# Kernel optimization log

Hardware: AMD Instinct MI355X
Metric: run time of the kernel (lower is better)

## Reference

```python
import jax, jax.numpy as jnp
import numpy as np

DIM = 256
NUM_HEADS = 8
HEAD_DIM = DIM // NUM_HEADS
WH, WW = 7, 7
N = WH * WW              # tokens per window = 49
NUM_WINDOWS = 64         # windows per image (56x56 map / 7x7 windows)
B_TOTAL = 2048           # num_windows * B_images
SCALE = HEAD_DIM ** -0.5


def _relative_position_index():
    # Matches the tf.meshgrid (xy indexing) construction in the source.
    coords = np.stack(np.meshgrid(np.arange(WH), np.arange(WW)), axis=0)  # [2, WW, WH]
    flat = coords.reshape(2, -1)                                          # [2, N]
    rel = flat[:, :, None] - flat[:, None, :]                             # [2, N, N]
    rel = rel.transpose(1, 2, 0).astype(np.int32)                         # [N, N, 2]
    rel[:, :, 0] += WH - 1
    rel[:, :, 1] += WW - 1
    rel[:, :, 0] *= 2 * WW - 1
    return rel.sum(-1)                                                    # [N, N]


def setup_inputs() -> dict:
    key = jax.random.key(0)
    ks = jax.random.split(key, 6)
    std = 0.02
    x = jax.random.normal(ks[0], (B_TOTAL, N, DIM), dtype=jnp.float32)
    mask = jnp.zeros((NUM_WINDOWS, N, N), dtype=jnp.float32)  # 0 / -inf additive mask
    qkv_w = jax.random.normal(ks[1], (DIM, 3 * DIM), dtype=jnp.float32) * std
    qkv_b = jnp.zeros((3 * DIM,), dtype=jnp.float32)
    proj_w = jax.random.normal(ks[2], (DIM, DIM), dtype=jnp.float32) * std
    proj_b = jnp.zeros((DIM,), dtype=jnp.float32)
    n_rel = (2 * WH - 1) * (2 * WW - 1)  # 169
    bias_table = jax.random.normal(ks[3], (n_rel, NUM_HEADS), dtype=jnp.float32) * std
    rel_index = jnp.asarray(_relative_position_index(), dtype=jnp.int32)
    return {"x": x, "mask": mask, "qkv_w": qkv_w, "qkv_b": qkv_b,
            "proj_w": proj_w, "proj_b": proj_b, "bias_table": bias_table,
            "rel_index": rel_index}


def reference(x, mask, qkv_w, qkv_b, proj_w, proj_b, bias_table, rel_index):
    B = x.shape[0]
    # qkv projection -> [3, B, H, N, hd]
    qkv = x @ qkv_w + qkv_b                                  # [B, N, 3C]
    qkv = qkv.reshape(B, N, 3, NUM_HEADS, HEAD_DIM)
    qkv = jnp.transpose(qkv, (2, 0, 3, 1, 4))
    q, k, v = qkv[0], qkv[1], qkv[2]
    # scaled attention scores [B, H, N, N]
    attn = jnp.einsum('bhnd,bhmd->bhnm', q, k) * SCALE
    # relative position bias gather: [N*N] -> [N, N, H] -> [1, H, N, N]
    bias = bias_table[rel_index.reshape(-1)].reshape(N, N, NUM_HEADS)
    attn = attn + jnp.transpose(bias, (2, 0, 1))[None]
    # additive window mask [nW, N, N]
    nW = mask.shape[0]
    attn = attn.reshape(B // nW, nW, NUM_HEADS, N, N) + mask[None, :, None]
    attn = attn.reshape(B, NUM_HEADS, N, N)
    attn = jax.nn.softmax(attn, axis=-1)
    out = jnp.einsum('bhnm,bhmd->bhnd', attn, v)             # [B, H, N, hd]
    out = jnp.transpose(out, (0, 2, 1, 3)).reshape(B, N, DIM)
    return out @ proj_w + proj_b
```

## Files before the change

kernel.cpp:

```cpp
#include <hip/hip_runtime.h>

#define NTOK 49
#define NHEAD 8
#define HDIM 32
#define DIMC 256
#define SCALE_F 0.17677669529663687f

typedef __attribute__((ext_vector_type(8))) short short8;
typedef __attribute__((ext_vector_type(4))) float f32x4;

#define AS1P(p) ((__attribute__((address_space(1))) void*)(p))
#define AS3P(p) ((__attribute__((address_space(3))) void*)(p))

__device__ inline unsigned short f2bf(float f) {
    unsigned int u = __float_as_uint(f);
    u += 0x7fffu + ((u >> 16) & 1u);
    return (unsigned short)(u >> 16);
}

__global__ __launch_bounds__(256) void conv_pack(const float* __restrict__ in,
    unsigned short* __restrict__ xp, int M)
{
    __shared__ __align__(16) unsigned short T[32 * 64 * 8];
    const int t = threadIdx.x;
    const size_t m0 = (size_t)blockIdx.x * 64;
    const float* src = in + m0 * 256;
    #pragma unroll
    for (int i = 0; i < 8; ++i) {
        const int li = i * 256 + t;
        const int r  = li >> 5;
        const int kc = li & 31;
        float4 a = ((const float4*)src)[li * 2];
        float4 b = ((const float4*)src)[li * 2 + 1];
        union { unsigned short s[8]; uint4 v; } u;
        u.s[0] = f2bf(a.x); u.s[1] = f2bf(a.y); u.s[2] = f2bf(a.z); u.s[3] = f2bf(a.w);
        u.s[4] = f2bf(b.x); u.s[5] = f2bf(b.y); u.s[6] = f2bf(b.z); u.s[7] = f2bf(b.w);
        *(uint4*)(T + kc * 512 + ((r ^ (kc & 7)) * 8)) = u.v;
    }
    __syncthreads();
    #pragma unroll
    for (int j = 0; j < 8; ++j) {
        const int li = j * 256 + t;
        const int kc = li >> 6;
        const int r  = li & 63;
        uint4 v = *(const uint4*)(T + kc * 512 + ((r ^ (kc & 7)) * 8));
        *(uint4*)(xp + ((size_t)kc * M + m0 + r) * 8) = v;
    }
}

__global__ __launch_bounds__(256) void pack_w(const float* __restrict__ W,
    unsigned short* __restrict__ Wp, int K, int N)
{
    int idx = blockIdx.x * 256 + threadIdx.x;
    if (idx >= K * N) return;
    int k = idx / N, n = idx - k * N;
    Wp[((size_t)(k >> 3) * N + n) * 8 + (k & 7)] = f2bf(W[idx]);
}

__global__ __launch_bounds__(256) void bm_build(const float* __restrict__ bias_table,
    const int* __restrict__ rel_index, const float* __restrict__ mask,
    float* __restrict__ bm)
{
    int idx = blockIdx.x * 256 + threadIdx.x;
    if (idx >= 64 * NHEAD * NTOK * NTOK) return;
    int wh = idx / (NTOK * NTOK);
    int ij = idx - wh * (NTOK * NTOK);
    int w = wh >> 3, h = wh & 7;
    bm[idx] = bias_table[rel_index[ij] * NHEAD + h] + mask[(size_t)w * (NTOK * NTOK) + ij];
}

__global__ __launch_bounds__(256) void gemm_mfma(
    const unsigned short* __restrict__ Ap,
    const unsigned short* __restrict__ Wp,
    const float* __restrict__ Bv,
    unsigned short* __restrict__ Yv,
    int N, int M, int nbm)
{
    __shared__ __align__(16) unsigned short As[4096];
    __shared__ __align__(16) unsigned short Bs[4096];

    const int tid  = threadIdx.x;
    const int lane = tid & 63;
    const int wv   = tid >> 6;
    const int quad = lane >> 4;
    const int l15  = lane & 15;

    const int nbn = N >> 7;
    const int lin = blockIdx.x;
    int mblk, nblk;
    if ((nbm & 7) == 0) {
        const int xcd = lin & 7;
        const int g   = lin >> 3;
        const int gm  = g / nbn;
        mblk = xcd * (nbm >> 3) + gm;
        nblk = g - gm * nbn;
    } else {
        mblk = lin / nbn;
        nblk = lin - mblk * nbn;
    }
    const long m0 = (long)mblk * 128;
    const int  n0 = nblk * 128;
    const int  wm = (wv >> 1) * 64;
    const int  wn = (wv & 1) * 64;

    const unsigned short* ga0 = Ap + ((size_t)wv * M + m0 + lane) * 8;
    const unsigned short* ga1 = ga0 + 64 * 8;
    const unsigned short* gb0 = Wp + ((size_t)wv * N + n0 + lane) * 8;
    const unsigned short* gb1 = gb0 + 64 * 8;

    f32x4 acc[4][4];
    #pragma unroll
    for (int i = 0; i < 4; ++i)
        #pragma unroll
        for (int j = 0; j < 4; ++j) acc[i][j] = (f32x4){0.f, 0.f, 0.f, 0.f};

    for (int k0 = 0; k0 < 256; k0 += 32) {
        const size_t aofs = (size_t)(k0 >> 3) * M * 8;
        const size_t bofs = (size_t)(k0 >> 3) * N * 8;
        __builtin_amdgcn_global_load_lds(AS1P(ga0 + aofs), AS3P(As + wv * 1024),       16, 0, 0);
        __builtin_amdgcn_global_load_lds(AS1P(ga1 + aofs), AS3P(As + wv * 1024 + 512), 16, 0, 0);
        __builtin_amdgcn_global_load_lds(AS1P(gb0 + bofs), AS3P(Bs + wv * 1024),       16, 0, 0);
        __builtin_amdgcn_global_load_lds(AS1P(gb1 + bofs), AS3P(Bs + wv * 1024 + 512), 16, 0, 0);
        __syncthreads();
        short8 af[4], bq[4];
        #pragma unroll
        for (int t = 0; t < 4; ++t) {
            af[t] = *(const short8*)(As + quad * 1024 + (wm + t * 16 + l15) * 8);
            bq[t] = *(const short8*)(Bs + quad * 1024 + (wn + t * 16 + l15) * 8);
        }
        #pragma unroll
        for (int ti = 0; ti < 4; ++ti)
            #pragma unroll
            for (int tj = 0; tj < 4; ++tj)
                acc[ti][tj] = __builtin_amdgcn_mfma_f32_16x16x32_bf16(bq[tj], af[ti], acc[ti][tj], 0, 0, 0);
        __syncthreads();
    }

    float4 bv4[4];
    #pragma unroll
    for (int tj = 0; tj < 4; ++tj)
        bv4[tj] = *(const float4*)(Bv + n0 + wn + tj * 16 + quad * 4);

    #pragma unroll
    for (int ti = 0; ti < 4; ++ti) {
        const long row = m0 + wm + ti * 16 + l15;
        #pragma unroll
        for (int tj = 0; tj < 4; ++tj) {
            const int col = n0 + wn + tj * 16 + quad * 4;
            uint2 u;
            u.x = (unsigned int)f2bf(acc[ti][tj][0] + bv4[tj].x)
                | ((unsigned int)f2bf(acc[ti][tj][1] + bv4[tj].y) << 16);
            u.y = (unsigned int)f2bf(acc[ti][tj][2] + bv4[tj].z)
                | ((unsigned int)f2bf(acc[ti][tj][3] + bv4[tj].w) << 16);
            *(uint2*)(Yv + row * N + col) = u;
        }
    }
}

__global__ __launch_bounds__(256) void attn_proj(
    const unsigned short* __restrict__ qkvb,
    const float* __restrict__ bm,
    const unsigned short* __restrict__ WpP,
    const float* __restrict__ Pb,
    float* __restrict__ outp,
    int win0)
{
    __shared__ __align__(16) unsigned short SMEM[4 * 3528 + 32 * 64 * 8];

    const int wv   = threadIdx.x >> 6;
    const int lane = threadIdx.x & 63;
    const int b    = blockIdx.x;
    const int w    = (win0 + b) & 63;
    const int quad = lane >> 4;
    const int l15  = lane & 15;

    unsigned short* Vt    = SMEM + wv * 3528;
    unsigned short* Ps    = SMEM + wv * 3528;
    unsigned short* O_lds = SMEM + 4 * 3528;

    #pragma unroll 1
    for (int hp = 0; hp < 2; ++hp) {
        const int h = wv * 2 + hp;
        const unsigned short* wbase = qkvb + (size_t)b * NTOK * 768 + h * HDIM;

        {
            const int tok = (lane < NTOK) ? lane : (NTOK - 1);
            const unsigned short* vp = wbase + (size_t)tok * 768 + 512;
            #pragma unroll
            for (int c = 0; c < 4; ++c) {
                uint4 vv = *(const uint4*)(vp + c * 8);
                unsigned int uu[4] = {vv.x, vv.y, vv.z, vv.w};
                #pragma unroll
                for (int e = 0; e < 4; ++e) {
                    int d = c * 8 + e * 2;
                    Vt[d * 72 + lane]       = (unsigned short)(uu[e] & 0xffffu);
                    Vt[(d + 1) * 72 + lane] = (unsigned short)(uu[e] >> 16);
                }
            }
        }

        short8 aq[4], bk[4];
        #pragma unroll
        for (int t = 0; t < 4; ++t) {
            int row = t * 16 + l15; if (row >= NTOK) row = NTOK - 1;
            const unsigned short* rp = wbase + (size_t)row * 768 + quad * 8;
            aq[t] = *(const short8*)(rp);
            bk[t] = *(const short8*)(rp + 256);
        }

        f32x4 sa[4][4];
        #pragma unroll
        for (int ti = 0; ti < 4; ++ti)
            #pragma unroll
            for (int tj = 0; tj < 4; ++tj) {
                f32x4 z = (f32x4){0.f, 0.f, 0.f, 0.f};
                sa[ti][tj] = __builtin_amdgcn_mfma_f32_16x16x32_bf16(aq[ti], bk[tj], z, 0, 0, 0);
            }

        short8 vb2[2][2];
        #pragma unroll
        for (int td = 0; td < 2; ++td)
            #pragma unroll
            for (int kc = 0; kc < 2; ++kc)
                vb2[td][kc] = *(const short8*)(Vt + (td * 16 + l15) * 72 + kc * 32 + quad * 8);

        const float* bmb = bm + (size_t)(w * NHEAD + h) * (NTOK * NTOK);
        float inv[4][4];
        #pragma unroll
        for (int ti = 0; ti < 4; ++ti) {
            #pragma unroll
            for (int r = 0; r < 4; ++r) {
                const int row = ti * 16 + quad * 4 + r;
                float sv[4];
                #pragma unroll
                for (int tj = 0; tj < 4; ++tj) {
                    const int col = tj * 16 + l15;
                    float s;
                    if (col < NTOK) {
                        float add = (row < NTOK) ? bmb[row * NTOK + col] : 0.f;
                        s = sa[ti][tj][r] * SCALE_F + add;
                    } else {
                        s = -__builtin_inff();
                    }
                    sv[tj] = s;
                }
                float e0 = __expf(sv[0]), e1 = __expf(sv[1]);
                float e2 = __expf(sv[2]), e3 = __expf(sv[3]);
                sa[ti][0][r] = e0; sa[ti][1][r] = e1; sa[ti][2][r] = e2; sa[ti][3][r] = e3;
                float sum = (e0 + e1) + (e2 + e3);
                sum += __shfl_xor(sum, 1, 16);
                sum += __shfl_xor(sum, 2, 16);
                sum += __shfl_xor(sum, 4, 16);
                sum += __shfl_xor(sum, 8, 16);
                inv[ti][r] = 1.f / sum;
            }
        }

        __syncthreads();

        #pragma unroll
        for (int ti = 0; ti < 4; ++ti)
            #pragma unroll
            for (int r = 0; r < 4; ++r) {
                const int row = ti * 16 + quad * 4 + r;
                if (row < NTOK) {
                    #pragma unroll
                    for (int tj = 0; tj < 4; ++tj)
                        Ps[row * 72 + tj * 16 + l15] = f2bf(sa[ti][tj][r]);
                }
            }

        short8 pa[4][2];
        #pragma unroll
        for (int ti = 0; ti < 4; ++ti) {
            int row = ti * 16 + l15; if (row >= NTOK) row = NTOK - 1;
            #pragma unroll
            for (int kc = 0; kc < 2; ++kc)
                pa[ti][kc] = *(const short8*)(Ps + row * 72 + kc * 32 + quad * 8);
        }
        f32x4 oa[4][2];
        #pragma unroll
        for (int ti = 0; ti < 4; ++ti)
            #pragma unroll
            for (int td = 0; td < 2; ++td) {
                f32x4 z = (f32x4){0.f, 0.f, 0.f, 0.f};
                z = __builtin_amdgcn_mfma_f32_16x16x32_bf16(pa[ti][0], vb2[td][0], z, 0, 0, 0);
                oa[ti][td] = __builtin_amdgcn_mfma_f32_16x16x32_bf16(pa[ti][1], vb2[td][1], z, 0, 0, 0);
            }

        #pragma unroll
        for (int ti = 0; ti < 4; ++ti)
            #pragma unroll
            for (int r = 0; r < 4; ++r) {
                const int row = ti * 16 + quad * 4 + r;
                if (row < NTOK) {
                    const float si = inv[ti][r];
                    #pragma unroll
                    for (int td = 0; td < 2; ++td) {
                        const int d = td * 16 + l15;
                        const int kc = h * 4 + (d >> 3);
                        O_lds[((size_t)kc * 64 + row) * 8 + (d & 7)] =
                            f2bf(oa[ti][td][r] * si);
                    }
                }
            }
    }

    __syncthreads();

    const int wn = wv * 64;
    f32x4 pacc[4][4];
    #pragma unroll
    for (int i = 0; i < 4; ++i)
        #pragma unroll
        for (int j = 0; j < 4; ++j) pacc[i][j] = (f32x4){0.f, 0.f, 0.f, 0.f};

    short8 pbq[4];
    #pragma unroll
    for (int t = 0; t < 4; ++t)
        pbq[t] = *(const short8*)(WpP + ((size_t)quad * 256 + wn + t * 16 + l15) * 8);

    #pragma unroll
    for (int K0 = 0; K0 < 8; ++K0) {
        short8 af[4], bq[4];
        #pragma unroll
        for (int t = 0; t < 4; ++t)
            af[t] = *(const short8*)(O_lds + ((size_t)(K0 * 4 + quad) * 64 + t * 16 + l15) * 8);
        #pragma unroll
        for (int t = 0; t < 4; ++t) bq[t] = pbq[t];
        if (K0 < 7) {
            #pragma unroll
            for (int t = 0; t < 4; ++t)
                pbq[t] = *(const short8*)(WpP + ((size_t)((K0 + 1) * 4 + quad) * 256 + wn + t * 16 + l15) * 8);
        }
        #pragma unroll
        for (int ti = 0; ti < 4; ++ti)
            #pragma unroll
            for (int tj = 0; tj < 4; ++tj)
                pacc[ti][tj] = __builtin_amdgcn_mfma_f32_16x16x32_bf16(bq[tj], af[ti], pacc[ti][tj], 0, 0, 0);
    }

    float4 bv4[4];
    #pragma unroll
    for (int tj = 0; tj < 4; ++tj)
        bv4[tj] = *(const float4*)(Pb + wn + tj * 16 + quad * 4);

    float* obase = outp + (size_t)b * NTOK * 256;
    #pragma unroll
    for (int ti = 0; ti < 4; ++ti) {
        const int row = ti * 16 + l15;
        if (row < NTOK) {
            #pragma unroll
            for (int tj = 0; tj < 4; ++tj) {
                const int col = wn + tj * 16 + quad * 4;
                float4 o = {pacc[ti][tj][0] + bv4[tj].x,
                            pacc[ti][tj][1] + bv4[tj].y,
                            pacc[ti][tj][2] + bv4[tj].z,
                            pacc[ti][tj][3] + bv4[tj].w};
                *(float4*)(obase + (size_t)row * 256 + col) = o;
            }
        }
    }
}

extern "C" void kernel_launch(void* const* d_in, const int* in_sizes, int n_in,
                              void* d_out, int out_size, void* d_ws, size_t ws_size,
                              hipStream_t stream)
{
    const float* x          = (const float*)d_in[0];
    const float* mask       = (const float*)d_in[1];
    const float* qkv_w      = (const float*)d_in[2];
    const float* qkv_b      = (const float*)d_in[3];
    const float* proj_w     = (const float*)d_in[4];
    const float* proj_b     = (const float*)d_in[5];
    const float* bias_table = (const float*)d_in[6];
    const int*   rel_index  = (const int*)d_in[7];
    float* outp = (float*)d_out;

    const int B_TOTAL = 2048;
    char* ws = (char*)d_ws;
    size_t off = 0;
    auto carve = [&](size_t bytes) -> void* {
        void* p = ws + off; off += (bytes + 255) & ~(size_t)255; return p;
    };
    unsigned short* WpQ = (unsigned short*)carve((size_t)256 * 768 * 2);
    unsigned short* WpP = (unsigned short*)carve((size_t)256 * 256 * 2);
    float* bm = (float*)carve((size_t)64 * NHEAD * NTOK * NTOK * 4);
    const size_t fixed = off;
    const size_t PER_WIN = (size_t)NTOK * 256 * 2 + (size_t)NTOK * 768 * 2;
    size_t avail = (ws_size > fixed + 1024) ? (ws_size - fixed - 1024) : 0;
    int chunkW = (int)(avail / PER_WIN);
    if (chunkW > B_TOTAL) chunkW = B_TOTAL;
    chunkW &= ~127;
    if (chunkW < 128) chunkW = 128;
    unsigned short* x_bf = (unsigned short*)carve((size_t)chunkW * NTOK * 256 * 2);
    unsigned short* qkvb = (unsigned short*)carve((size_t)chunkW * NTOK * 768 * 2);

    pack_w<<<(256 * 768 + 255) / 256, 256, 0, stream>>>(qkv_w, WpQ, 256, 768);
    pack_w<<<(256 * 256 + 255) / 256, 256, 0, stream>>>(proj_w, WpP, 256, 256);
    bm_build<<<(64 * NHEAD * NTOK * NTOK + 255) / 256, 256, 0, stream>>>(
        bias_table, rel_index, mask, bm);

    for (int w0 = 0; w0 < B_TOTAL; w0 += chunkW) {
        int wc = B_TOTAL - w0; if (wc > chunkW) wc = chunkW;
        const int Mc = wc * NTOK;
        const int nbm = Mc / 128;
        conv_pack<<<Mc / 64, 256, 0, stream>>>(
            x + (size_t)w0 * NTOK * DIMC, x_bf, Mc);
        gemm_mfma<<<dim3(nbm * 6), 256, 0, stream>>>(x_bf, WpQ, qkv_b, qkvb, 768, Mc, nbm);
        attn_proj<<<dim3(wc), 256, 0, stream>>>(
            qkvb, bm, WpP, proj_b, outp + (size_t)w0 * NTOK * DIMC, w0);
    }
}
```

Baseline: 448.0 us.

## Alias per-wave attention scratch with O tile in LDS to raise occupancy

The separate O_lds staging area is removed and overlaid on the per-wave V/P scratch region, roughly halving the kernel's shared memory so more blocks can fit on a CU. Normalized attention outputs are packed to bf16 in registers for both heads and written to LDS only after a single block barrier. The in-loop __syncthreads is replaced by a wave-local lgkmcnt wait, and launch bounds request 3 blocks per CU. The trade-off is extra live registers (ost array plus full unroll of the head loop), which could cause spills or limit occupancy in other ways.

```diff
diff --git a/kernel.cpp b/kernel.cpp
--- a/kernel.cpp
+++ b/kernel.cpp
@@ -157,7 +157,7 @@
     }
 }
 
-__global__ __launch_bounds__(256) void attn_proj(
+__global__ __launch_bounds__(256, 3) void attn_proj(
     const unsigned short* __restrict__ qkvb,
     const float* __restrict__ bm,
     const unsigned short* __restrict__ WpP,
@@ -165,7 +165,7 @@
     float* __restrict__ outp,
     int win0)
 {
-    __shared__ __align__(16) unsigned short SMEM[4 * 3528 + 32 * 64 * 8];
+    __shared__ __align__(16) unsigned short SMEM[32 * 64 * 8];
 
     const int wv   = threadIdx.x >> 6;
     const int lane = threadIdx.x & 63;
@@ -176,9 +176,11 @@
 
     unsigned short* Vt    = SMEM + wv * 3528;
     unsigned short* Ps    = SMEM + wv * 3528;
-    unsigned short* O_lds = SMEM + 4 * 3528;
-
-    #pragma unroll 1
+    unsigned short* O_lds = SMEM;
+
+    unsigned int ost[2][4][2][2];
+
+    #pragma unroll
     for (int hp = 0; hp < 2; ++hp) {
         const int h = wv * 2 + hp;
         const unsigned short* wbase = qkvb + (size_t)b * NTOK * 768 + h * HDIM;
@@ -223,6 +225,7 @@
             #pragma unroll
             for (int kc = 0; kc < 2; ++kc)
                 vb2[td][kc] = *(const short8*)(Vt + (td * 16 + l15) * 72 + kc * 32 + quad * 8);
+        asm volatile("s_waitcnt lgkmcnt(0)" ::: "memory");
 
         const float* bmb = bm + (size_t)(w * NHEAD + h) * (NTOK * NTOK);
         float inv[4][4];
@@ -256,8 +259,6 @@
             }
         }
 
-        __syncthreads();
-
         #pragma unroll
         for (int ti = 0; ti < 4; ++ti)
             #pragma unroll
@@ -291,16 +292,33 @@
         #pragma unroll
         for (int ti = 0; ti < 4; ++ti)
             #pragma unroll
+            for (int td = 0; td < 2; ++td) {
+                ost[hp][ti][td][0] =
+                    (unsigned int)f2bf(oa[ti][td][0] * inv[ti][0])
+                  | ((unsigned int)f2bf(oa[ti][td][1] * inv[ti][1]) << 16);
+                ost[hp][ti][td][1] =
+                    (unsigned int)f2bf(oa[ti][td][2] * inv[ti][2])
+                  | ((unsigned int)f2bf(oa[ti][td][3] * inv[ti][3]) << 16);
+            }
+    }
+
+    __syncthreads();
+
+    #pragma unroll
+    for (int hp = 0; hp < 2; ++hp) {
+        const int h = wv * 2 + hp;
+        #pragma unroll
+        for (int ti = 0; ti < 4; ++ti)
+            #pragma unroll
             for (int r = 0; r < 4; ++r) {
                 const int row = ti * 16 + quad * 4 + r;
                 if (row < NTOK) {
-                    const float si = inv[ti][r];
                     #pragma unroll
                     for (int td = 0; td < 2; ++td) {
-                        const int d = td * 16 + l15;
+                        const int d  = td * 16 + l15;
                         const int kc = h * 4 + (d >> 3);
-                        O_lds[((size_t)kc * 64 + row) * 8 + (d & 7)] =
-                            f2bf(oa[ti][td][r] * si);
+                        O_lds[(size_t)kc * 512 + row * 8 + (d & 7)] =
+                            (unsigned short)(ost[hp][ti][td][r >> 1] >> (16 * (r & 1)));
                     }
                 }
             }
```

Result: faster. 408.2 us (-8.9%).
